# Performance work log

Hardware: AMD Instinct MI355X
Metric: run time of the kernel (lower is better)

## Reference

```python
import jax, jax.numpy as jnp
import numpy as np

B, L, F, D = 128, 64, 3072, 1024
CV, CN = 512, 1024  # verb/noun concept channels
MAX_K = (L + 7) // 8
BN_EPS = 1e-5


def setup_inputs() -> dict:
    key = jax.random.key(0)
    ks = jax.random.split(key, 24)
    s_in = 1.0 / np.sqrt(F)
    s_d = 1.0 / np.sqrt(D)
    inp = {
        'inputs': jax.random.normal(ks[0], (B, L, F), jnp.float32),
        'input_lens': jax.random.randint(ks[1], (B,), 1, L + 1, jnp.int32),
        # three level linear embeds
        'W0': jax.random.normal(ks[2], (F, D), jnp.float32) * s_in,
        'b0': jnp.zeros((D,), jnp.float32),
        'W1': jax.random.normal(ks[3], (F, D), jnp.float32) * s_in,
        'b1': jnp.zeros((D,), jnp.float32),
        'W2': jax.random.normal(ks[4], (F, D), jnp.float32) * s_in,
        'b2': jnp.zeros((D,), jnp.float32),
        # attention scorer
        'w_attn': jax.random.normal(ks[5], (D, 1), jnp.float32) * s_d,
        'b_attn': jnp.zeros((1,), jnp.float32),
        # verb classifier: Conv1d(D, CV, 3, pad=1) + BN + sigmoid
        'Kv': jax.random.normal(ks[6], (CV, D, 3), jnp.float32) * (1.0 / np.sqrt(D * 3)),
        'bv': jnp.zeros((CV,), jnp.float32),
        'g_v': jnp.ones((CV,), jnp.float32),
        'beta_v': jnp.zeros((CV,), jnp.float32),
        'mean_v': jax.random.normal(ks[7], (CV,), jnp.float32) * 0.1,
        'var_v': jax.random.uniform(ks[8], (CV,), jnp.float32, 0.5, 1.5),
        # noun classifier: Conv1d(D, CN, 1) + BN + sigmoid
        'Kn': jax.random.normal(ks[9], (CN, D, 1), jnp.float32) * s_d,
        'bn_b': jnp.zeros((CN,), jnp.float32),
        'g_n': jnp.ones((CN,), jnp.float32),
        'beta_n': jnp.zeros((CN,), jnp.float32),
        'mean_n': jax.random.normal(ks[10], (CN,), jnp.float32) * 0.1,
        'var_n': jax.random.uniform(ks[11], (CN,), jnp.float32, 0.5, 1.5),
    }
    return inp


def _conv_bn_sigmoid(x_bld, K, b, gamma, beta, mean, var, pad):
    # x_bld: (B, L, D) -> permute to NCH (B, D, L) as in torch
    x = jnp.transpose(x_bld, (0, 2, 1))
    y = jax.lax.conv_general_dilated(
        x, K, window_strides=(1,), padding=[(pad, pad)],
        dimension_numbers=('NCH', 'OIH', 'NCH'))
    y = y + b[None, :, None]
    # BatchNorm1d in eval mode (running stats)
    y = (y - mean[None, :, None]) * jax.lax.rsqrt(var + BN_EPS)[None, :, None]
    y = y * gamma[None, :, None] + beta[None, :, None]
    y = jax.nn.sigmoid(y)
    return jnp.transpose(y, (0, 2, 1))  # (B, L, C)


def _topk_mean(logits, input_lens):
    # logits: (B, L, C); per-sample top-ceil(len/8) over time, then mean
    lens = input_lens.astype(jnp.int32)
    kk = (lens + 7) // 8  # (B,)
    valid = (jnp.arange(L)[None, :] < lens[:, None])  # (B, L)
    masked = jnp.where(valid[:, :, None], logits, -1e18)
    # top MAX_K per (batch, class) over time
    top = jax.lax.top_k(jnp.transpose(masked, (0, 2, 1)), MAX_K)[0]  # (B, C, MAX_K)
    take = (jnp.arange(MAX_K)[None, None, :] < kk[:, None, None]).astype(logits.dtype)
    return jnp.sum(top * take, axis=-1) / kk[:, None].astype(logits.dtype)  # (B, C)


def reference(inputs, input_lens, W0, b0, W1, b1, W2, b2, w_attn, b_attn,
              Kv, bv, g_v, beta_v, mean_v, var_v,
              Kn, bn_b, g_n, beta_n, mean_n, var_n):
    # level embeds (dropout is identity in eval)
    e0 = inputs @ W0 + b0
    e1 = inputs @ W1 + b1
    e2 = inputs @ W2 + b2

    # masked softmax attention pooling over time -> sent_embeds
    scores = (e0 @ w_attn)[:, :, 0] + b_attn[0]  # (B, L)
    valid = jnp.arange(L)[None, :] < input_lens[:, None]
    scores = jnp.where(valid, scores, -1e18)
    attn = jax.nn.softmax(scores, axis=1)
    sent_embeds = jnp.sum(e0 * attn[:, :, None], axis=1)  # (B, D)

    logits_verb = _conv_bn_sigmoid(e1, Kv, bv, g_v, beta_v, mean_v, var_v, pad=1)  # (B, L, CV)
    logits_noun = _conv_bn_sigmoid(e2, Kn, bn_b, g_n, beta_n, mean_n, var_n, pad=0)  # (B, L, CN)

    instance_logits_verb = _topk_mean(logits_verb, input_lens)  # (B, CV)
    instance_logits_noun = _topk_mean(logits_noun, input_lens)  # (B, CN)

    return (sent_embeds, e1, e2, instance_logits_verb, instance_logits_noun)
```

## Files before the change

kernel.cpp:

```cpp
#include <hip/hip_runtime.h>
#include <cstdint>
#include <cstddef>

typedef unsigned short u16;
typedef __attribute__((ext_vector_type(8))) short short8;
typedef __attribute__((ext_vector_type(4))) float f32x4;

static __device__ __forceinline__ float bf2f(u16 h) {
  union { unsigned u; float f; } a; a.u = ((unsigned)h) << 16; return a.f;
}
static __device__ __forceinline__ u16 f2bf(float x) {
  union { float f; unsigned u; } a; a.f = x;
  return (u16)((a.u + 0x7fffu + ((a.u >> 16) & 1u)) >> 16);
}

#define GLDS16(gp, lp)                                                          \
  __builtin_amdgcn_global_load_lds(                                             \
      (const __attribute__((address_space(1))) void*)(gp),                      \
      (__attribute__((address_space(3))) void*)(lp), 16, 0, 0)

template<int N> static __device__ __forceinline__ void vmwait() {
  if constexpr (N == 0)      asm volatile("s_waitcnt vmcnt(0)" ::: "memory");
  else if constexpr (N == 3) asm volatile("s_waitcnt vmcnt(3)" ::: "memory");
  else if constexpr (N == 4) asm volatile("s_waitcnt vmcnt(4)" ::: "memory");
  else if constexpr (N == 6) asm volatile("s_waitcnt vmcnt(6)" ::: "memory");
  else if constexpr (N == 8) asm volatile("s_waitcnt vmcnt(8)" ::: "memory");
}

__global__ void prep_all(const float* __restrict__ inputs, u16* __restrict__ Xbf,
                         const float* __restrict__ W0, const float* __restrict__ W1,
                         const float* __restrict__ W2, u16* __restrict__ Wt,
                         const float* __restrict__ Kv, const float* __restrict__ bv,
                         const float* __restrict__ g_v, const float* __restrict__ beta_v,
                         const float* __restrict__ mean_v, const float* __restrict__ var_v,
                         u16* __restrict__ KVt, float* __restrict__ biasv,
                         const float* __restrict__ Kn, const float* __restrict__ bnb,
                         const float* __restrict__ g_n, const float* __restrict__ beta_n,
                         const float* __restrict__ mean_n, const float* __restrict__ var_n,
                         u16* __restrict__ KNt, float* __restrict__ biasn,
                         u16* __restrict__ e1pad) {
  __shared__ float tile[32][33];
  const int id = blockIdx.x;
  const int tid = threadIdx.x;
  if (id < 2048) {
    int i = id * 256 + tid;
#pragma unroll
    for (int it = 0; it < 12; it++) {
      float4 v = ((const float4*)inputs)[i];
      ushort4 o;
      o.x = f2bf(v.x); o.y = f2bf(v.y); o.z = f2bf(v.z); o.w = f2bf(v.w);
      ((ushort4*)Xbf)[i] = o;
      i += 2048 * 256;
    }
  } else if (id < 2816) {
    const int tx = tid & 31, ty = tid >> 5;
    for (int it = 0; it < 12; it++) {
      const int tl = (id - 2048) + 768 * it;
      const int kb = (tl % 96) * 32;
      const int jb = (tl / 96) * 32;
      const int w = jb >> 10;
      const float* W = (w == 0) ? W0 : ((w == 1) ? W1 : W2);
      const int nb = jb & 1023;
#pragma unroll
      for (int i = 0; i < 4; i++)
        tile[ty + 8 * i][tx] = W[(size_t)(kb + ty + 8 * i) * 1024 + nb + tx];
      __syncthreads();
#pragma unroll
      for (int i = 0; i < 4; i++)
        Wt[(size_t)(jb + ty + 8 * i) * 3072 + kb + tx] = f2bf(tile[tx][ty + 8 * i]);
      __syncthreads();
    }
  } else if (id < 3328) {
    const int c = id - 2816;
    const float scale = g_v[c] * rsqrtf(var_v[c] + 1e-5f);
    for (int t = 0; t < 3; t++)
      for (int d = tid; d < 1024; d += 256)
        KVt[(size_t)c * 3072 + t * 1024 + d] = f2bf(Kv[(size_t)c * 3072 + d * 3 + t] * scale);
    if (tid == 0) biasv[c] = (bv[c] - mean_v[c]) * scale + beta_v[c];
  } else if (id < 4352) {
    const int c = id - 3328;
    const float scale = g_n[c] * rsqrtf(var_n[c] + 1e-5f);
    for (int d = tid; d < 1024; d += 256)
      KNt[(size_t)c * 1024 + d] = f2bf(Kn[(size_t)c * 1024 + d] * scale);
    if (tid == 0) biasn[c] = (bnb[c] - mean_n[c]) * scale + beta_n[c];
  } else {
    const int i = (id - 4352) * 256 + tid;
    const int b = i >> 11;
    const int j = i & 2047;
    const int r = (j < 1024) ? 0 : 65;
    const int d = j & 1023;
    e1pad[(size_t)(b * 66 + r) * 1024 + d] = 0;
  }
}


#define STAGE_(NSL, KO)                                                         \
  {                                                                             \
    const size_t ko_ = (KO);                                                    \
    GLDS16(gA + ko_, stA + (NSL) * SLOTU);                                      \
    _Pragma("unroll")                                                           \
    for (int g = 0; g < NBG; g++)                                               \
      GLDS16(gB + (size_t)g * gBgrp + ko_, stB + (NSL) * SLOTU + g * 4096);     \
  }

#define BODY_(SL, NSL, T, DOSTAGE, VM)                                          \
  {                                                                             \
    const u16* ra = rdA + (SL) * SLOTU + pA;                                    \
    const u16* rb = rdB + (SL) * SLOTU + pA;                                    \
    short8 fa[4];                                                               \
    short8 fb[FJ];                                                              \
    _Pragma("unroll")                                                           \
    for (int i = 0; i < 4; i++) fa[i] = *(const short8*)(ra + i * 512);         \
    _Pragma("unroll")                                                           \
    for (int j = 0; j < FJ; j++) fb[j] = *(const short8*)(rb + j * 512);        \
    if (DOSTAGE) STAGE_(NSL, (size_t)((T) + 3) * 32);                           \
    __builtin_amdgcn_s_barrier();                                               \
    __builtin_amdgcn_s_setprio(1);                                              \
    _Pragma("unroll")                                                           \
    for (int i = 0; i < 4; i++)                                                 \
      _Pragma("unroll")                                                         \
      for (int j = 0; j < FJ; j++)                                              \
        acc[i][j] = __builtin_amdgcn_mfma_f32_16x16x32_bf16(fa[i], fb[j],       \
                                                            acc[i][j], 0, 0, 0);\
    __builtin_amdgcn_s_setprio(0);                                              \
    vmwait<VM>();                                                               \
    __builtin_amdgcn_s_barrier();                                               \
  }

template<int FJv, int NT>
static __device__ __forceinline__ void gemm_pipe(
    const u16* __restrict__ gA, const u16* __restrict__ gB, const size_t gBgrp,
    u16* lds, f32x4 (*acc)[FJv]) {
  constexpr int FJ = FJv;
  constexpr int SLOTU = 4096 + FJ * 2048;
  constexpr int NBG = FJ / 2;
  constexpr int G = 1 + NBG;
  const int tid = threadIdx.x;
  const int lane = tid & 63;
  const int warp = tid >> 6;
  const int wm = warp & 1, wn = warp >> 1;
  const int l15 = lane & 15, quad = lane >> 4;
  u16* stA = lds + tid * 8;
  u16* stB = lds + 4096 + tid * 8;
  const u16* rdA = lds + (wm * 64 + l15) * 32;
  const u16* rdB = lds + 4096 + (wn * (FJ * 16) + l15) * 32;
  const int pA = ((quad + (l15 >> 1)) & 3) * 8;

  STAGE_(0, 0);
  STAGE_(1, 32);
  STAGE_(2, 64);
  vmwait<2 * G>();
  __builtin_amdgcn_s_barrier();

  int t = 0;
#pragma unroll 1
  for (; t < NT - 4; t += 4) {
    BODY_(0, 3, t,     true, 2 * G);
    BODY_(1, 0, t + 1, true, 2 * G);
    BODY_(2, 1, t + 2, true, 2 * G);
    BODY_(3, 2, t + 3, true, 2 * G);
  }
  BODY_(0, 3, t,     true,  2 * G);
  BODY_(1, 0, t + 1, false, G);
  BODY_(2, 1, t + 2, false, 0);
  BODY_(3, 2, t + 3, false, 63);
}

static __device__ __forceinline__ void topk_epilogue(
    f32x4 (*acc)[4], const float* __restrict__ bias,
    const int* __restrict__ lens, float* __restrict__ out,
    const int NC, const int m0, const int n0) {
  const int tid = threadIdx.x;
  const int lane = tid & 63;
  const int warp = tid >> 6;
  const int wm = warp & 1, wn = warp >> 1;
  const int l15 = lane & 15, quad = lane >> 4;
  const int b = (m0 >> 6) + wm;
  const int len = lens[b];
  const int kk8 = (len + 7) >> 3;
#pragma unroll
  for (int j = 0; j < 4; j++) {
    const int c = n0 + wn * 64 + j * 16 + l15;
    const float bias_c = bias[c];
    float t[8];
#pragma unroll
    for (int q8 = 0; q8 < 8; q8++) t[q8] = -1e30f;
#pragma unroll
    for (int i = 0; i < 4; i++) {
#pragma unroll
      for (int r = 0; r < 4; r++) {
        const int l = i * 16 + quad * 4 + r;
        const float v = acc[i][j][r] + bias_c;
        const float sg = 1.0f / (1.0f + __expf(-v));
        float x = (l < len) ? sg : -1e30f;
#pragma unroll
        for (int q8 = 0; q8 < 8; q8++) {
          const float hi = fmaxf(t[q8], x);
          x = fminf(t[q8], x);
          t[q8] = hi;
        }
      }
    }
#pragma unroll
    for (int mask = 16; mask <= 32; mask <<= 1) {
      float xs[8];
#pragma unroll
      for (int q8 = 0; q8 < 8; q8++) xs[q8] = __shfl_xor(t[q8], mask);
#pragma unroll
      for (int q8 = 0; q8 < 8; q8++) {
        float x = xs[q8];
#pragma unroll
        for (int p8 = 0; p8 < 8; p8++) {
          const float hi = fmaxf(t[p8], x);
          x = fminf(t[p8], x);
          t[p8] = hi;
        }
      }
    }
    if (quad == 0) {
      float s = 0.f;
#pragma unroll
      for (int q8 = 0; q8 < 8; q8++) s += (q8 < kk8) ? t[q8] : 0.f;
      out[(size_t)b * NC + c] = s / (float)kk8;
    }
  }
}

__global__ __launch_bounds__(512, 2) void gemm_embed(
    const u16* __restrict__ A, const u16* __restrict__ Bmat,
    const float* __restrict__ bias0, const float* __restrict__ bias1,
    const float* __restrict__ bias2,
    float* __restrict__ oute1, float* __restrict__ oute2,
    u16* __restrict__ e0bf, u16* __restrict__ e1pad, u16* __restrict__ e2bf) {
  __shared__ __align__(16) u16 lds[4 * (4096 + 6 * 2048)];
  const int tid = threadIdx.x;
  const int m0 = blockIdx.y * 128;
  const int n0 = blockIdx.x * 384;
  const int u = tid >> 2;
  const int cs = (((tid & 3) - (tid >> 3)) & 3) * 8;

  f32x4 acc[4][6];
#pragma unroll
  for (int i = 0; i < 4; i++)
#pragma unroll
    for (int j = 0; j < 6; j++) acc[i][j] = (f32x4){0.f, 0.f, 0.f, 0.f};

  gemm_pipe<6, 96>(A + (size_t)(m0 + u) * 3072 + cs,
                   Bmat + (size_t)(n0 + u) * 3072 + cs, (size_t)128 * 3072,
                   lds, acc);

  const int lane = tid & 63;
  const int warp = tid >> 6;
  const int wm = warp & 1, wn = warp >> 1;
  const int l15 = lane & 15, quad = lane >> 4;
#pragma unroll
  for (int j = 0; j < 6; j++) {
    const int cb = n0 + wn * 96 + j * 16;
    const int w = cb >> 10;
    const int n = (cb & 1023) + l15;
    const float bias = ((w == 0) ? bias0 : (w == 1) ? bias1 : bias2)[n];
#pragma unroll
    for (int i = 0; i < 4; i++) {
      const int mr = m0 + wm * 64 + i * 16 + quad * 4;
#pragma unroll
      for (int r = 0; r < 4; r++) {
        const int m = mr + r;
        const float v = acc[i][j][r] + bias;
        if (w == 0) {
          e0bf[(size_t)m * 1024 + n] = f2bf(v);
        } else if (w == 1) {
          oute1[(size_t)m * 1024 + n] = v;
          e1pad[(size_t)((m >> 6) * 66 + (m & 63) + 1) * 1024 + n] = f2bf(v);
        } else {
          oute2[(size_t)m * 1024 + n] = v;
          e2bf[(size_t)m * 1024 + n] = f2bf(v);
        }
      }
    }
  }
}

__global__ __launch_bounds__(512, 2) void fused_tail(
    const u16* __restrict__ e1pad, const u16* __restrict__ KVt,
    const float* __restrict__ biasv,
    const u16* __restrict__ e2bf, const u16* __restrict__ KNt,
    const float* __restrict__ biasn,
    const u16* __restrict__ e0bf, const float* __restrict__ w_attn,
    const float* __restrict__ b_attn, const int* __restrict__ lens,
    float* __restrict__ out_sent, float* __restrict__ out_ilv,
    float* __restrict__ out_iln) {
  __shared__ __align__(16) u16 smem[4 * (4096 + 4 * 2048)];
  const int id = blockIdx.x;
  const int tid = threadIdx.x;
  if (id < 384) {
    const int u = tid >> 2;
    const int cs = (((tid & 3) - (tid >> 3)) & 3) * 8;
    f32x4 acc[4][4];
#pragma unroll
    for (int i = 0; i < 4; i++)
#pragma unroll
      for (int j = 0; j < 4; j++) acc[i][j] = (f32x4){0.f, 0.f, 0.f, 0.f};
    if (id < 128) {
      const int by = id >> 1, bx = id & 1;
      const int n0 = bx * 256;
      const int rowoff = (u < 64) ? u : (u + 2);
      gemm_pipe<4, 96>(e1pad + ((size_t)(by * 2) * 66 + rowoff) * 1024 + cs,
                       KVt + (size_t)(n0 + u) * 3072 + cs, (size_t)128 * 3072,
                       smem, acc);
      topk_epilogue(acc, biasv, lens, out_ilv, 512, by * 128, n0);
    } else {
      const int id2 = id - 128;
      const int by = id2 >> 2, bx = id2 & 3;
      const int m0 = by * 128, n0 = bx * 256;
      gemm_pipe<4, 32>(e2bf + (size_t)(m0 + u) * 1024 + cs,
                       KNt + (size_t)(n0 + u) * 1024 + cs, (size_t)128 * 1024,
                       smem, acc);
      topk_epilogue(acc, biasn, lens, out_iln, 1024, m0, n0);
    }
  } else {
    const int b = id - 384;
    const int lane = tid & 63;
    const int warp = tid >> 6;
    float* sc = (float*)smem;
    float* at = sc + 64;
    const int len = lens[b];
    if (warp < 4) {
      for (int t = 0; t < 16; t++) {
        const int l = warp * 16 + t;
        const u16* row = e0bf + (size_t)(b * 64 + l) * 1024;
        float s = 0.f;
#pragma unroll
        for (int uu = 0; uu < 16; uu++) {
          const int d = lane + uu * 64;
          s += bf2f(row[d]) * w_attn[d];
        }
#pragma unroll
        for (int off = 32; off > 0; off >>= 1) s += __shfl_down(s, off);
        if (lane == 0) sc[l] = s + b_attn[0];
      }
    }
    __syncthreads();
    if (warp == 0) {
      float v = (lane < len) ? sc[lane] : -1e30f;
      float m = v;
#pragma unroll
      for (int off = 32; off > 0; off >>= 1) m = fmaxf(m, __shfl_xor(m, off));
      float p = (lane < len) ? __expf(v - m) : 0.f;
      float ssum = p;
#pragma unroll
      for (int off = 32; off > 0; off >>= 1) ssum += __shfl_xor(ssum, off);
      at[lane] = p / ssum;
    }
    __syncthreads();
    if (tid < 256) {
      const int d0 = tid * 4;
      float a0 = 0.f, a1 = 0.f, a2 = 0.f, a3 = 0.f;
      for (int l = 0; l < 64; l++) {
        const float wgt = at[l];
        const ushort4 u4 = *(const ushort4*)(e0bf + (size_t)(b * 64 + l) * 1024 + d0);
        a0 += wgt * bf2f(u4.x);
        a1 += wgt * bf2f(u4.y);
        a2 += wgt * bf2f(u4.z);
        a3 += wgt * bf2f(u4.w);
      }
      float4 o; o.x = a0; o.y = a1; o.z = a2; o.w = a3;
      *(float4*)(out_sent + (size_t)b * 1024 + d0) = o;
    }
  }
}

extern "C" void kernel_launch(void* const* d_in, const int* in_sizes, int n_in,
                              void* d_out, int out_size, void* d_ws, size_t ws_size,
                              hipStream_t stream) {
  const float* inputs = (const float*)d_in[0];
  const int*   lens   = (const int*)d_in[1];
  const float* W0 = (const float*)d_in[2];
  const float* b0 = (const float*)d_in[3];
  const float* W1 = (const float*)d_in[4];
  const float* b1 = (const float*)d_in[5];
  const float* W2 = (const float*)d_in[6];
  const float* b2 = (const float*)d_in[7];
  const float* w_attn = (const float*)d_in[8];
  const float* b_attn = (const float*)d_in[9];
  const float* Kv   = (const float*)d_in[10];
  const float* bv   = (const float*)d_in[11];
  const float* g_v  = (const float*)d_in[12];
  const float* beta_v = (const float*)d_in[13];
  const float* mean_v = (const float*)d_in[14];
  const float* var_v  = (const float*)d_in[15];
  const float* Kn   = (const float*)d_in[16];
  const float* bn_b = (const float*)d_in[17];
  const float* g_n  = (const float*)d_in[18];
  const float* beta_n = (const float*)d_in[19];
  const float* mean_n = (const float*)d_in[20];
  const float* var_n  = (const float*)d_in[21];

  float* out = (float*)d_out;
  float* out_sent = out;
  float* out_e1   = out + 131072;
  float* out_e2   = out + 131072 + 8388608;
  float* out_ilv  = out + 131072 + 2 * 8388608;
  float* out_iln  = out_ilv + 65536;

  char* p = (char*)d_ws;
  u16* Xbf  = (u16*)p; p += (size_t)8192 * 3072 * 2;
  u16* Wt   = (u16*)p; p += (size_t)3072 * 3072 * 2;
  u16* KVt  = (u16*)p; p += (size_t)512 * 3072 * 2;
  u16* KNt  = (u16*)p; p += (size_t)1024 * 1024 * 2;
  float* biasv = (float*)p; p += 512 * 4;
  float* biasn = (float*)p; p += 1024 * 4;
  u16* e0bf  = (u16*)p; p += (size_t)8192 * 1024 * 2;
  u16* e1pad = (u16*)p; p += (size_t)128 * 66 * 1024 * 2;
  u16* e2bf  = (u16*)p; p += (size_t)8192 * 1024 * 2;

  prep_all<<<5376, 256, 0, stream>>>(inputs, Xbf, W0, W1, W2, Wt,
                                     Kv, bv, g_v, beta_v, mean_v, var_v, KVt, biasv,
                                     Kn, bn_b, g_n, beta_n, mean_n, var_n, KNt, biasn,
                                     e1pad);
  gemm_embed<<<dim3(8, 64), 512, 0, stream>>>(Xbf, Wt, b0, b1, b2, out_e1, out_e2,
                                              e0bf, e1pad, e2bf);
  fused_tail<<<512, 512, 0, stream>>>(e1pad, KVt, biasv, e2bf, KNt, biasn,
                                      e0bf, w_attn, b_attn, lens,
                                      out_sent, out_ilv, out_iln);
}
```

Baseline: 497.1 us.

## Restructure GEMM pipeline to 4-warp 128x256 tiles with 3-slot split-phase staging

Replaces the 8-warp gemm_pipe (4-slot LDS ring, 128x384 or 128x256 tiles) with a 4-warp gemm_core. Each warp owns all 128 rows and a 64-column slice, and the LDS ring drops to 3 slots. Each k-step is split into two halves, each interleaving half the global->LDS loads with MFMAs, and the conv im2col row remapping moves inside the core. The aim is less LDS traffic per MFMA (B fragments reused across 8 row tiles) and smaller LDS use. In exchange it doubles accumulator registers per thread, which can hurt occupancy, and uses a shallower prefetch depth.

```diff
diff --git a/kernel.cpp b/kernel.cpp
--- a/kernel.cpp
+++ b/kernel.cpp
@@ -21,10 +21,7 @@
 
 template<int N> static __device__ __forceinline__ void vmwait() {
   if constexpr (N == 0)      asm volatile("s_waitcnt vmcnt(0)" ::: "memory");
-  else if constexpr (N == 3) asm volatile("s_waitcnt vmcnt(3)" ::: "memory");
-  else if constexpr (N == 4) asm volatile("s_waitcnt vmcnt(4)" ::: "memory");
   else if constexpr (N == 6) asm volatile("s_waitcnt vmcnt(6)" ::: "memory");
-  else if constexpr (N == 8) asm volatile("s_waitcnt vmcnt(8)" ::: "memory");
 }
 
 __global__ void prep_all(const float* __restrict__ inputs, u16* __restrict__ Xbf,
@@ -93,77 +90,112 @@
   }
 }
 
-
-#define STAGE_(NSL, KO)                                                         \
+#define SLOTU 12288
+
+#define STG_H0(SL, K)                                                           \
+  { GLDS16(srcA0 + (K), dA0 + (SL) * SLOTU);                                    \
+    GLDS16(srcA1 + (K), dA1 + (SL) * SLOTU);                                    \
+    GLDS16(srcB0 + (K), dB0 + (SL) * SLOTU); }
+#define STG_H1(SL, K)                                                           \
+  { GLDS16(srcB1 + (K), dB1 + (SL) * SLOTU);                                    \
+    GLDS16(srcB2 + (K), dB2 + (SL) * SLOTU);                                    \
+    GLDS16(srcB3 + (K), dB3 + (SL) * SLOTU); }
+
+#define BODY_(SL, NSL, T)                                                       \
   {                                                                             \
-    const size_t ko_ = (KO);                                                    \
-    GLDS16(gA + ko_, stA + (NSL) * SLOTU);                                      \
+    const int t_ = (T);                                                         \
+    const bool st_ = (t_ + 2 < NT);                                             \
+    const size_t k2_ = (size_t)(t_ + 2) * 32;                                   \
+    const u16* ra = rdA + (SL) * SLOTU;                                         \
+    const u16* rb = rdB + (SL) * SLOTU;                                         \
+    short8 fa[4], fb[4];                                                        \
     _Pragma("unroll")                                                           \
-    for (int g = 0; g < NBG; g++)                                               \
-      GLDS16(gB + (size_t)g * gBgrp + ko_, stB + (NSL) * SLOTU + g * 4096);     \
-  }
-
-#define BODY_(SL, NSL, T, DOSTAGE, VM)                                          \
-  {                                                                             \
-    const u16* ra = rdA + (SL) * SLOTU + pA;                                    \
-    const u16* rb = rdB + (SL) * SLOTU + pA;                                    \
-    short8 fa[4];                                                               \
-    short8 fb[FJ];                                                              \
+    for (int j = 0; j < 4; j++) fb[j] = *(const short8*)(rb + j * 512);         \
     _Pragma("unroll")                                                           \
     for (int i = 0; i < 4; i++) fa[i] = *(const short8*)(ra + i * 512);         \
-    _Pragma("unroll")                                                           \
-    for (int j = 0; j < FJ; j++) fb[j] = *(const short8*)(rb + j * 512);        \
-    if (DOSTAGE) STAGE_(NSL, (size_t)((T) + 3) * 32);                           \
+    if (st_) STG_H0(NSL, k2_);                                                  \
     __builtin_amdgcn_s_barrier();                                               \
     __builtin_amdgcn_s_setprio(1);                                              \
     _Pragma("unroll")                                                           \
     for (int i = 0; i < 4; i++)                                                 \
       _Pragma("unroll")                                                         \
-      for (int j = 0; j < FJ; j++)                                              \
+      for (int j = 0; j < 4; j++)                                               \
         acc[i][j] = __builtin_amdgcn_mfma_f32_16x16x32_bf16(fa[i], fb[j],       \
                                                             acc[i][j], 0, 0, 0);\
     __builtin_amdgcn_s_setprio(0);                                              \
-    vmwait<VM>();                                                               \
     __builtin_amdgcn_s_barrier();                                               \
-  }
-
-template<int FJv, int NT>
-static __device__ __forceinline__ void gemm_pipe(
-    const u16* __restrict__ gA, const u16* __restrict__ gB, const size_t gBgrp,
-    u16* lds, f32x4 (*acc)[FJv]) {
-  constexpr int FJ = FJv;
-  constexpr int SLOTU = 4096 + FJ * 2048;
-  constexpr int NBG = FJ / 2;
-  constexpr int G = 1 + NBG;
+    _Pragma("unroll")                                                           \
+    for (int i = 0; i < 4; i++) fa[i] = *(const short8*)(ra + 2048 + i * 512);  \
+    if (st_) STG_H1(NSL, k2_);                                                  \
+    __builtin_amdgcn_s_barrier();                                               \
+    __builtin_amdgcn_s_setprio(1);                                              \
+    _Pragma("unroll")                                                           \
+    for (int i = 0; i < 4; i++)                                                 \
+      _Pragma("unroll")                                                         \
+      for (int j = 0; j < 4; j++)                                               \
+        acc[4 + i][j] = __builtin_amdgcn_mfma_f32_16x16x32_bf16(fa[i], fb[j],   \
+                                                      acc[4 + i][j], 0, 0, 0);  \
+    __builtin_amdgcn_s_setprio(0);                                              \
+    if (t_ < NT - 2) vmwait<6>();                                               \
+    else if (t_ == NT - 2) vmwait<0>();                                         \
+    __builtin_amdgcn_s_barrier();                                               \
+  }
+
+template<int NT, bool IM2COL>
+static __device__ __forceinline__ void gemm_core(
+    const u16* __restrict__ Abase, const int ldA,
+    const u16* __restrict__ Bbase, const int ldB,
+    u16* lds, f32x4 (*acc)[4]) {
   const int tid = threadIdx.x;
-  const int lane = tid & 63;
-  const int warp = tid >> 6;
-  const int wm = warp & 1, wn = warp >> 1;
-  const int l15 = lane & 15, quad = lane >> 4;
-  u16* stA = lds + tid * 8;
-  u16* stB = lds + 4096 + tid * 8;
-  const u16* rdA = lds + (wm * 64 + l15) * 32;
-  const u16* rdB = lds + 4096 + (wn * (FJ * 16) + l15) * 32;
-  const int pA = ((quad + (l15 >> 1)) & 3) * 8;
-
-  STAGE_(0, 0);
-  STAGE_(1, 32);
-  STAGE_(2, 64);
-  vmwait<2 * G>();
+  const int l = tid & 63;
+  const int w = tid >> 6;
+  const int l15 = l & 15, quad = l >> 4;
+  const int lr = l >> 2;
+  const int lpos = l & 3;
+
+  const u16 *srcA0, *srcA1, *srcB0, *srcB1, *srcB2, *srcB3;
+  u16 *dA0, *dA1, *dB0, *dB1, *dB2, *dB3;
+  {
+    const int r0 = (0 * 4 + w) * 16 + lr;
+    const int r1 = (1 * 4 + w) * 16 + lr;
+    const int c0 = (lpos - (r0 >> 1)) & 3;
+    const int c1 = (lpos - (r1 >> 1)) & 3;
+    const int rr0 = IM2COL ? (r0 + 2 * (r0 >> 6)) : r0;
+    const int rr1 = IM2COL ? (r1 + 2 * (r1 >> 6)) : r1;
+    srcA0 = Abase + (size_t)rr0 * ldA + c0 * 8;
+    srcA1 = Abase + (size_t)rr1 * ldA + c1 * 8;
+    dA0 = lds + (0 * 4 + w) * 512;
+    dA1 = lds + (1 * 4 + w) * 512;
+  }
+#pragma unroll
+  for (int g = 0; g < 4; g++) {
+    const int r = (g * 4 + w) * 16 + lr;
+    const int c = (lpos - (r >> 1)) & 3;
+    const u16* s = Bbase + (size_t)r * ldB + c * 8;
+    u16* d = lds + 4096 + (g * 4 + w) * 512;
+    if (g == 0) { srcB0 = s; dB0 = d; }
+    else if (g == 1) { srcB1 = s; dB1 = d; }
+    else if (g == 2) { srcB2 = s; dB2 = d; }
+    else { srcB3 = s; dB3 = d; }
+  }
+  const int psw = ((quad + (l15 >> 1)) & 3) * 8;
+  const u16* rdA = lds + l15 * 32 + psw;
+  const u16* rdB = lds + 4096 + (w * 64 + l15) * 32 + psw;
+
+  STG_H0(0, 0); STG_H1(0, 0);
+  STG_H0(1, 32); STG_H1(1, 32);
+  vmwait<6>();
   __builtin_amdgcn_s_barrier();
 
   int t = 0;
 #pragma unroll 1
-  for (; t < NT - 4; t += 4) {
-    BODY_(0, 3, t,     true, 2 * G);
-    BODY_(1, 0, t + 1, true, 2 * G);
-    BODY_(2, 1, t + 2, true, 2 * G);
-    BODY_(3, 2, t + 3, true, 2 * G);
-  }
-  BODY_(0, 3, t,     true,  2 * G);
-  BODY_(1, 0, t + 1, false, G);
-  BODY_(2, 1, t + 2, false, 0);
-  BODY_(3, 2, t + 3, false, 63);
+  for (; t + 3 <= NT; t += 3) {
+    BODY_(0, 2, t);
+    BODY_(1, 0, t + 1);
+    BODY_(2, 1, t + 2);
+  }
+  if constexpr (NT % 3 == 2) { BODY_(0, 2, NT - 2); BODY_(1, 0, NT - 1); }
+  else if constexpr (NT % 3 == 1) { BODY_(0, 2, NT - 1); }
 }
 
 static __device__ __forceinline__ void topk_epilogue(
@@ -171,97 +203,95 @@
     const int* __restrict__ lens, float* __restrict__ out,
     const int NC, const int m0, const int n0) {
   const int tid = threadIdx.x;
-  const int lane = tid & 63;
-  const int warp = tid >> 6;
-  const int wm = warp & 1, wn = warp >> 1;
-  const int l15 = lane & 15, quad = lane >> 4;
-  const int b = (m0 >> 6) + wm;
-  const int len = lens[b];
-  const int kk8 = (len + 7) >> 3;
-#pragma unroll
-  for (int j = 0; j < 4; j++) {
-    const int c = n0 + wn * 64 + j * 16 + l15;
-    const float bias_c = bias[c];
-    float t[8];
-#pragma unroll
-    for (int q8 = 0; q8 < 8; q8++) t[q8] = -1e30f;
-#pragma unroll
-    for (int i = 0; i < 4; i++) {
-#pragma unroll
-      for (int r = 0; r < 4; r++) {
-        const int l = i * 16 + quad * 4 + r;
-        const float v = acc[i][j][r] + bias_c;
-        const float sg = 1.0f / (1.0f + __expf(-v));
-        float x = (l < len) ? sg : -1e30f;
-#pragma unroll
-        for (int q8 = 0; q8 < 8; q8++) {
-          const float hi = fmaxf(t[q8], x);
-          x = fminf(t[q8], x);
-          t[q8] = hi;
+  const int l = tid & 63;
+  const int wn = tid >> 6;
+  const int l15 = l & 15, quad = l >> 4;
+#pragma unroll
+  for (int bs = 0; bs < 2; bs++) {
+    const int b = (m0 >> 6) + bs;
+    const int len = lens[b];
+    const int kk8 = (len + 7) >> 3;
+#pragma unroll
+    for (int j = 0; j < 4; j++) {
+      const int c = n0 + wn * 64 + j * 16 + l15;
+      const float bias_c = bias[c];
+      float t[8];
+#pragma unroll
+      for (int q8 = 0; q8 < 8; q8++) t[q8] = -1e30f;
+#pragma unroll
+      for (int i2 = 0; i2 < 4; i2++) {
+#pragma unroll
+        for (int r = 0; r < 4; r++) {
+          const int lrow = i2 * 16 + quad * 4 + r;
+          const float v = acc[bs * 4 + i2][j][r] + bias_c;
+          const float sg = 1.0f / (1.0f + __expf(-v));
+          float x = (lrow < len) ? sg : -1e30f;
+#pragma unroll
+          for (int q8 = 0; q8 < 8; q8++) {
+            const float hi = fmaxf(t[q8], x);
+            x = fminf(t[q8], x);
+            t[q8] = hi;
+          }
         }
       }
-    }
-#pragma unroll
-    for (int mask = 16; mask <= 32; mask <<= 1) {
-      float xs[8];
-#pragma unroll
-      for (int q8 = 0; q8 < 8; q8++) xs[q8] = __shfl_xor(t[q8], mask);
-#pragma unroll
-      for (int q8 = 0; q8 < 8; q8++) {
-        float x = xs[q8];
-#pragma unroll
-        for (int p8 = 0; p8 < 8; p8++) {
-          const float hi = fmaxf(t[p8], x);
-          x = fminf(t[p8], x);
-          t[p8] = hi;
+#pragma unroll
+      for (int mask = 16; mask <= 32; mask <<= 1) {
+        float xs[8];
+#pragma unroll
+        for (int q8 = 0; q8 < 8; q8++) xs[q8] = __shfl_xor(t[q8], mask);
+#pragma unroll
+        for (int q8 = 0; q8 < 8; q8++) {
+          float x = xs[q8];
+#pragma unroll
+          for (int p8 = 0; p8 < 8; p8++) {
+            const float hi = fmaxf(t[p8], x);
+            x = fminf(t[p8], x);
+            t[p8] = hi;
+          }
         }
       }
-    }
-    if (quad == 0) {
-      float s = 0.f;
-#pragma unroll
-      for (int q8 = 0; q8 < 8; q8++) s += (q8 < kk8) ? t[q8] : 0.f;
-      out[(size_t)b * NC + c] = s / (float)kk8;
-    }
-  }
-}
-
-__global__ __launch_bounds__(512, 2) void gemm_embed(
+      if (quad == 0) {
+        float s = 0.f;
+#pragma unroll
+        for (int q8 = 0; q8 < 8; q8++) s += (q8 < kk8) ? t[q8] : 0.f;
+        out[(size_t)b * NC + c] = s / (float)kk8;
+      }
+    }
+  }
+}
+
+__global__ __launch_bounds__(256, 2) void gemm_embed(
     const u16* __restrict__ A, const u16* __restrict__ Bmat,
     const float* __restrict__ bias0, const float* __restrict__ bias1,
     const float* __restrict__ bias2,
     float* __restrict__ oute1, float* __restrict__ oute2,
     u16* __restrict__ e0bf, u16* __restrict__ e1pad, u16* __restrict__ e2bf) {
-  __shared__ __align__(16) u16 lds[4 * (4096 + 6 * 2048)];
+  __shared__ __align__(16) u16 lds[3 * SLOTU];
+  const int m0 = blockIdx.y * 128;
+  const int n0 = blockIdx.x * 256;
+
+  f32x4 acc[8][4];
+#pragma unroll
+  for (int i = 0; i < 8; i++)
+#pragma unroll
+    for (int j = 0; j < 4; j++) acc[i][j] = (f32x4){0.f, 0.f, 0.f, 0.f};
+
+  gemm_core<96, false>(A + (size_t)m0 * 3072, 3072,
+                       Bmat + (size_t)n0 * 3072, 3072, lds, acc);
+
   const int tid = threadIdx.x;
-  const int m0 = blockIdx.y * 128;
-  const int n0 = blockIdx.x * 384;
-  const int u = tid >> 2;
-  const int cs = (((tid & 3) - (tid >> 3)) & 3) * 8;
-
-  f32x4 acc[4][6];
-#pragma unroll
-  for (int i = 0; i < 4; i++)
-#pragma unroll
-    for (int j = 0; j < 6; j++) acc[i][j] = (f32x4){0.f, 0.f, 0.f, 0.f};
-
-  gemm_pipe<6, 96>(A + (size_t)(m0 + u) * 3072 + cs,
-                   Bmat + (size_t)(n0 + u) * 3072 + cs, (size_t)128 * 3072,
-                   lds, acc);
-
-  const int lane = tid & 63;
-  const int warp = tid >> 6;
-  const int wm = warp & 1, wn = warp >> 1;
-  const int l15 = lane & 15, quad = lane >> 4;
-#pragma unroll
-  for (int j = 0; j < 6; j++) {
-    const int cb = n0 + wn * 96 + j * 16;
+  const int l = tid & 63;
+  const int wn = tid >> 6;
+  const int l15 = l & 15, quad = l >> 4;
+#pragma unroll
+  for (int j = 0; j < 4; j++) {
+    const int cb = n0 + wn * 64 + j * 16;
     const int w = cb >> 10;
     const int n = (cb & 1023) + l15;
     const float bias = ((w == 0) ? bias0 : (w == 1) ? bias1 : bias2)[n];
 #pragma unroll
-    for (int i = 0; i < 4; i++) {
-      const int mr = m0 + wm * 64 + i * 16 + quad * 4;
+    for (int i = 0; i < 8; i++) {
+      const int mr = m0 + i * 16 + quad * 4;
 #pragma unroll
       for (int r = 0; r < 4; r++) {
         const int m = mr + r;
@@ -280,7 +310,7 @@
   }
 }
 
-__global__ __launch_bounds__(512, 2) void fused_tail(
+__global__ __launch_bounds__(256, 2) void fused_tail(
     const u16* __restrict__ e1pad, const u16* __restrict__ KVt,
     const float* __restrict__ biasv,
     const u16* __restrict__ e2bf, const u16* __restrict__ KNt,
@@ -289,32 +319,27 @@
     const float* __restrict__ b_attn, const int* __restrict__ lens,
     float* __restrict__ out_sent, float* __restrict__ out_ilv,
     float* __restrict__ out_iln) {
-  __shared__ __align__(16) u16 smem[4 * (4096 + 4 * 2048)];
+  __shared__ __align__(16) u16 smem[3 * SLOTU];
   const int id = blockIdx.x;
   const int tid = threadIdx.x;
   if (id < 384) {
-    const int u = tid >> 2;
-    const int cs = (((tid & 3) - (tid >> 3)) & 3) * 8;
-    f32x4 acc[4][4];
-#pragma unroll
-    for (int i = 0; i < 4; i++)
+    f32x4 acc[8][4];
+#pragma unroll
+    for (int i = 0; i < 8; i++)
 #pragma unroll
       for (int j = 0; j < 4; j++) acc[i][j] = (f32x4){0.f, 0.f, 0.f, 0.f};
     if (id < 128) {
       const int by = id >> 1, bx = id & 1;
       const int n0 = bx * 256;
-      const int rowoff = (u < 64) ? u : (u + 2);
-      gemm_pipe<4, 96>(e1pad + ((size_t)(by * 2) * 66 + rowoff) * 1024 + cs,
-                       KVt + (size_t)(n0 + u) * 3072 + cs, (size_t)128 * 3072,
-                       smem, acc);
+      gemm_core<96, true>(e1pad + (size_t)(by * 2) * 66 * 1024, 1024,
+                          KVt + (size_t)n0 * 3072, 3072, smem, acc);
       topk_epilogue(acc, biasv, lens, out_ilv, 512, by * 128, n0);
     } else {
       const int id2 = id - 128;
       const int by = id2 >> 2, bx = id2 & 3;
       const int m0 = by * 128, n0 = bx * 256;
-      gemm_pipe<4, 32>(e2bf + (size_t)(m0 + u) * 1024 + cs,
-                       KNt + (size_t)(n0 + u) * 1024 + cs, (size_t)128 * 1024,
-                       smem, acc);
+      gemm_core<32, false>(e2bf + (size_t)m0 * 1024, 1024,
+                           KNt + (size_t)n0 * 1024, 1024, smem, acc);
       topk_epilogue(acc, biasn, lens, out_iln, 1024, m0, n0);
     }
   } else {
@@ -324,20 +349,18 @@
     float* sc = (float*)smem;
     float* at = sc + 64;
     const int len = lens[b];
-    if (warp < 4) {
-      for (int t = 0; t < 16; t++) {
-        const int l = warp * 16 + t;
-        const u16* row = e0bf + (size_t)(b * 64 + l) * 1024;
-        float s = 0.f;
-#pragma unroll
-        for (int uu = 0; uu < 16; uu++) {
-          const int d = lane + uu * 64;
-          s += bf2f(row[d]) * w_attn[d];
-        }
-#pragma unroll
-        for (int off = 32; off > 0; off >>= 1) s += __shfl_down(s, off);
-        if (lane == 0) sc[l] = s + b_attn[0];
+    for (int t = 0; t < 16; t++) {
+      const int lrow = warp * 16 + t;
+      const u16* row = e0bf + (size_t)(b * 64 + lrow) * 1024;
+      float s = 0.f;
+#pragma unroll
+      for (int uu = 0; uu < 16; uu++) {
+        const int d = lane + uu * 64;
+        s += bf2f(row[d]) * w_attn[d];
       }
+#pragma unroll
+      for (int off = 32; off > 0; off >>= 1) s += __shfl_down(s, off);
+      if (lane == 0) sc[lrow] = s + b_attn[0];
     }
     __syncthreads();
     if (warp == 0) {
@@ -352,20 +375,18 @@
       at[lane] = p / ssum;
     }
     __syncthreads();
-    if (tid < 256) {
-      const int d0 = tid * 4;
-      float a0 = 0.f, a1 = 0.f, a2 = 0.f, a3 = 0.f;
-      for (int l = 0; l < 64; l++) {
-        const float wgt = at[l];
-        const ushort4 u4 = *(const ushort4*)(e0bf + (size_t)(b * 64 + l) * 1024 + d0);
-        a0 += wgt * bf2f(u4.x);
-        a1 += wgt * bf2f(u4.y);
-        a2 += wgt * bf2f(u4.z);
-        a3 += wgt * bf2f(u4.w);
-      }
-      float4 o; o.x = a0; o.y = a1; o.z = a2; o.w = a3;
-      *(float4*)(out_sent + (size_t)b * 1024 + d0) = o;
-    }
+    const int d0 = tid * 4;
+    float a0 = 0.f, a1 = 0.f, a2 = 0.f, a3 = 0.f;
+    for (int lrow = 0; lrow < 64; lrow++) {
+      const float wgt = at[lrow];
+      const ushort4 u4 = *(const ushort4*)(e0bf + (size_t)(b * 64 + lrow) * 1024 + d0);
+      a0 += wgt * bf2f(u4.x);
+      a1 += wgt * bf2f(u4.y);
+      a2 += wgt * bf2f(u4.z);
+      a3 += wgt * bf2f(u4.w);
+    }
+    float4 o; o.x = a0; o.y = a1; o.z = a2; o.w = a3;
+    *(float4*)(out_sent + (size_t)b * 1024 + d0) = o;
   }
 }
 
@@ -417,9 +438,9 @@
                                      Kv, bv, g_v, beta_v, mean_v, var_v, KVt, biasv,
                                      Kn, bn_b, g_n, beta_n, mean_n, var_n, KNt, biasn,
                                      e1pad);
-  gemm_embed<<<dim3(8, 64), 512, 0, stream>>>(Xbf, Wt, b0, b1, b2, out_e1, out_e2,
-                                              e0bf, e1pad, e2bf);
-  fused_tail<<<512, 512, 0, stream>>>(e1pad, KVt, biasv, e2bf, KNt, biasn,
+  gemm_embed<<<dim3(12, 64), 256, 0, stream>>>(Xbf, Wt, b0, b1, b2, out_e1, out_e2,
+                                               e0bf, e1pad, e2bf);
+  fused_tail<<<512, 256, 0, stream>>>(e1pad, KVt, biasv, e2bf, KNt, biasn,
                                       e0bf, w_attn, b_attn, lens,
                                       out_sent, out_ilv, out_iln);
 }
```

Result: no change. 506.4 us (+1.9%).
